# Performance work log

Hardware: AMD Instinct MI355X
Metric: run time of the kernel (lower is better)

## Reference

```python
import jax, jax.numpy as jnp
import numpy as np

N_NODES = 50000


def gcn_conv(x, edge_index, W, b, n_nodes):
    """GCNConv: out = D^-1/2 (A + I) D^-1/2 (x W) + b (symmetric norm, self-loops)."""
    src, dst = edge_index[0], edge_index[1]
    loop = jnp.arange(n_nodes, dtype=src.dtype)
    src = jnp.concatenate([src, loop])  # [E + N]
    dst = jnp.concatenate([dst, loop])
    deg = jax.ops.segment_sum(jnp.ones_like(dst, dtype=x.dtype), dst,
                              num_segments=n_nodes)
    dinv = jnp.where(deg > 0, jax.lax.rsqrt(deg), 0.0)
    norm = dinv[src] * dinv[dst]  # [E + N]
    h = x @ W  # [N, out_dim]
    msg = h[src] * norm[:, None]  # gather + scale, [E + N, out_dim]
    out = jax.ops.segment_sum(msg, dst, num_segments=n_nodes)  # scatter-add
    return out + b


def batch_norm(x, gamma, beta, eps=1e-5):
    mean = jnp.mean(x, axis=0)
    var = jnp.var(x, axis=0)
    return (x - mean) * jax.lax.rsqrt(var + eps) * gamma + beta


def setup_inputs() -> dict:
    key = jax.random.key(0)
    ks = jax.random.split(key, 6)
    in_c, hid, lat = 64, 128, 64
    x = jax.random.normal(ks[0], (N_NODES, in_c), dtype=jnp.float32)
    edge_index = jax.random.randint(ks[1], (2, 1600000), 0, N_NODES, dtype=jnp.int64)
    W1 = jax.random.normal(ks[2], (in_c, hid), dtype=jnp.float32) * (1.0 / np.sqrt(in_c))
    b1 = jnp.zeros((hid,), dtype=jnp.float32)
    gamma = jnp.ones((hid,), dtype=jnp.float32)
    beta = jnp.zeros((hid,), dtype=jnp.float32)
    W2 = jax.random.normal(ks[3], (hid, lat), dtype=jnp.float32) * (1.0 / np.sqrt(hid))
    b2 = jnp.zeros((lat,), dtype=jnp.float32)
    return {"x": x, "edge_index": edge_index, "W1": W1, "b1": b1,
            "gamma": gamma, "beta": beta, "W2": W2, "b2": b2}


def reference(x, edge_index, W1, b1, gamma, beta, W2, b2):
    h = gcn_conv(x, edge_index, W1, b1, N_NODES)
    h = batch_norm(h, gamma, beta)
    h = jax.nn.relu(h)
    # dropout omitted (deterministic reference; identity in expectation-free eval)
    return gcn_conv(h, edge_index, W2, b2, N_NODES)
```

## Files before the change

### kernel.cpp

```cpp
#include <hip/hip_runtime.h>

#define N_NODES 50000
#define C1 64
#define C2 128
#define C3 64
#define NBUCK ((N_NODES + 63) / 64)
#define BCAP 8192
#define STILE 4096

__device__ __forceinline__ float bf2f(unsigned short u) {
    union { unsigned int i; float f; } v; v.i = ((unsigned int)u) << 16; return v.f;
}
__device__ __forceinline__ unsigned short f2bf(float f) {
    union { float f; unsigned int i; } v; v.f = f;
    return (unsigned short)((v.i + 0x7FFFu + ((v.i >> 16) & 1u)) >> 16);
}

__global__ void k_zero_cast(const float* __restrict__ x, unsigned short* __restrict__ xh,
                            int* __restrict__ bcount, float* __restrict__ stats) {
    int i = blockIdx.x * blockDim.x + threadIdx.x;
    if (i < NBUCK) bcount[i] = 0;
    if (i < 512) stats[i] = 0.0f;
    if (i < N_NODES * C1 / 4) {
        float4 v = ((const float4*)x)[i];
        ushort4 o;
        o.x = f2bf(v.x); o.y = f2bf(v.y); o.z = f2bf(v.z); o.w = f2bf(v.w);
        ((ushort4*)xh)[i] = o;
    }
}

__global__ __launch_bounds__(256) void k_hist(const int* __restrict__ dst, int E,
                                              int* __restrict__ bcount) {
    __shared__ int lh[NBUCK];
    int tid = threadIdx.x;
    for (int i = tid; i < NBUCK; i += 256) lh[i] = 0;
    __syncthreads();
    int stride = gridDim.x * blockDim.x;
    for (int e = blockIdx.x * blockDim.x + tid; e < E; e += stride)
        atomicAdd(&lh[dst[e] >> 6], 1);
    __syncthreads();
    for (int i = tid; i < NBUCK; i += 256)
        if (lh[i]) atomicAdd(&bcount[i], lh[i]);
}

__global__ __launch_bounds__(1024) void k_scanb(const int* __restrict__ bcount,
                                                int* __restrict__ bstart,
                                                int* __restrict__ bcursor) {
    __shared__ int sums[1024];
    int t = threadIdx.x;
    int v = (t < NBUCK) ? bcount[t] : 0;
    sums[t] = v;
    __syncthreads();
    for (int off = 1; off < 1024; off <<= 1) {
        int u = (t >= off) ? sums[t - off] : 0;
        __syncthreads();
        sums[t] += u;
        __syncthreads();
    }
    if (t < NBUCK) {
        int ex = sums[t] - v;
        bstart[t] = ex;
        bcursor[t * 16] = ex;
    }
}

__global__ __launch_bounds__(256) void k_scatterc(const int* __restrict__ src,
                                                  const int* __restrict__ dst, int E,
                                                  int* __restrict__ bcursor,
                                                  int* __restrict__ pairs) {
    __shared__ int lh[NBUCK];
    __shared__ int gbase[NBUCK];
    int tid = threadIdx.x;
    int base = blockIdx.x * STILE;
    for (int i = tid; i < NBUCK; i += 256) lh[i] = 0;
    __syncthreads();
    int sv[16], dv[16], rk[16];
#pragma unroll
    for (int k = 0; k < 16; ++k) {
        int e = base + k * 256 + tid;
        sv[k] = -1;
        if (e < E) {
            sv[k] = src[e];
            dv[k] = dst[e];
            rk[k] = atomicAdd(&lh[dv[k] >> 6], 1);
        }
    }
    __syncthreads();
    for (int i = tid; i < NBUCK; i += 256) {
        int c = lh[i];
        gbase[i] = c ? atomicAdd(&bcursor[i * 16], c) : 0;
    }
    __syncthreads();
#pragma unroll
    for (int k = 0; k < 16; ++k) {
        if (sv[k] >= 0) {
            int b = dv[k] >> 6;
            pairs[gbase[b] + rk[k]] = (sv[k] << 6) | (dv[k] & 63);
        }
    }
}

__global__ __launch_bounds__(256) void k_refine(const int* __restrict__ bstart,
                                                const int* __restrict__ bcount,
                                                int* __restrict__ rowstart,
                                                float* __restrict__ dinv,
                                                int* __restrict__ pairs) {
    __shared__ int stage[BCAP];
    __shared__ int lcnt[64];
    __shared__ int lcur[64];
    int b = blockIdx.x;
    int tid = threadIdx.x;
    int e0 = bstart[b], n = bcount[b];
    if (tid < 64) lcnt[tid] = 0;
    __syncthreads();
    for (int j = tid; j < n; j += 256) {
        int pk = pairs[e0 + j];
        stage[j] = pk;
        atomicAdd(&lcnt[pk & 63], 1);
    }
    __syncthreads();
    if (tid < 64) {
        int dg = lcnt[tid];
        int pfx = dg;
#pragma unroll
        for (int off = 1; off < 64; off <<= 1) {
            int v = __shfl_up(pfx, off);
            if (tid >= off) pfx += v;
        }
        int st = e0 + (pfx - dg);
        int nd = b * 64 + tid;
        rowstart[nd] = st;
        dinv[nd] = rsqrtf(1.0f + (float)dg);
        lcur[tid] = st;
    }
    __syncthreads();
    for (int j = tid; j < n; j += 256) {
        int pk = stage[j];
        int pos = atomicAdd(&lcur[pk & 63], 1);
        pairs[pos] = pk >> 6;
    }
}

__global__ __launch_bounds__(256) void k_pullx(const int* __restrict__ rowstart,
                                               const int* __restrict__ csr,
                                               const float* __restrict__ x,
                                               const unsigned short* __restrict__ xh,
                                               const float* __restrict__ dinv,
                                               float* __restrict__ aggx) {
    int node = blockIdx.x * 4 + (threadIdx.x >> 6);
    if (node >= N_NODES) return;
    int lane = threadIdx.x & 63;
    int start = rowstart[node], end = rowstart[node + 1];
    float dd = dinv[node];
    float acc = x[node * C1 + lane] * dd * dd;
    for (int j0 = start; j0 < end; j0 += 64) {
        int n = end - j0; if (n > 64) n = 64;
        int idx = 0;
        if (lane < n) idx = csr[j0 + lane];
        float ds = dinv[idx];
        int k = 0;
        for (; k + 3 < n; k += 4) {
            int s0 = __shfl(idx, k),     s1 = __shfl(idx, k + 1);
            int s2 = __shfl(idx, k + 2), s3 = __shfl(idx, k + 3);
            float w0 = __shfl(ds, k) * dd,     w1 = __shfl(ds, k + 1) * dd;
            float w2 = __shfl(ds, k + 2) * dd, w3 = __shfl(ds, k + 3) * dd;
            float v0 = bf2f(xh[s0 * C1 + lane]), v1 = bf2f(xh[s1 * C1 + lane]);
            float v2 = bf2f(xh[s2 * C1 + lane]), v3 = bf2f(xh[s3 * C1 + lane]);
            acc = fmaf(v0, w0, acc); acc = fmaf(v1, w1, acc);
            acc = fmaf(v2, w2, acc); acc = fmaf(v3, w3, acc);
        }
        for (; k < n; ++k) {
            int s = __shfl(idx, k);
            float w = __shfl(ds, k) * dd;
            acc = fmaf(bf2f(xh[s * C1 + lane]), w, acc);
        }
    }
    aggx[node * C1 + lane] = acc;
}

__global__ __launch_bounds__(256) void k_gemm1b(const float* __restrict__ aggx,
                                                const float* __restrict__ W1,
                                                const float* __restrict__ b1,
                                                float* __restrict__ agg1) {
    __shared__ float Ws[C1 * C2];
    __shared__ float Xs[32 * C1];
    int tid = threadIdx.x;
    int r0 = blockIdx.x * 32;
    for (int i = tid; i < C1 * C2; i += 256) Ws[i] = W1[i];
    for (int i = tid; i < 32 * C1; i += 256) {
        int row = r0 + (i >> 6);
        Xs[i] = (row < N_NODES) ? aggx[row * C1 + (i & 63)] : 0.0f;
    }
    __syncthreads();
    int c = tid & 127;
    int rg = tid >> 7;
    float bv = b1[c];
    float acc[16];
#pragma unroll
    for (int r = 0; r < 16; ++r) acc[r] = 0.0f;
    for (int k = 0; k < C1; ++k) {
        float w = Ws[k * C2 + c];
#pragma unroll
        for (int r = 0; r < 16; ++r)
            acc[r] = fmaf(Xs[(rg * 16 + r) * C1 + k], w, acc[r]);
    }
#pragma unroll
    for (int r = 0; r < 16; ++r) {
        int row = r0 + rg * 16 + r;
        if (row < N_NODES) agg1[row * C2 + c] = acc[r] + bv;
    }
}

__global__ __launch_bounds__(256) void k_stats(const float* __restrict__ agg1,
                                               float* __restrict__ stats) {
    __shared__ float ls[256], lq[256];
    int tid = threadIdx.x;
    int c = tid & 127, half = tid >> 7;
    float s = 0.0f, q = 0.0f;
    for (int row = blockIdx.x * 2 + half; row < N_NODES; row += gridDim.x * 2) {
        float v = agg1[row * C2 + c];
        s += v; q += v * v;
    }
    ls[tid] = s; lq[tid] = q;
    __syncthreads();
    if (tid < 128) {
        s = ls[tid] + ls[tid + 128];
        q = lq[tid] + lq[tid + 128];
        unsafeAtomicAdd(&stats[c], s);
        unsafeAtomicAdd(&stats[128 + c], q);
    }
}

__global__ void k_bnparam(const float* __restrict__ gamma, const float* __restrict__ beta,
                          float* __restrict__ stats) {
    int c = threadIdx.x;
    if (c < 128) {
        const float invN = 1.0f / (float)N_NODES;
        float mean = stats[c] * invN;
        float var = stats[128 + c] * invN - mean * mean;
        float sc = gamma[c] * rsqrtf(var + 1e-5f);
        stats[256 + c] = sc;
        stats[384 + c] = beta[c] - mean * sc;
    }
}

__global__ __launch_bounds__(256) void k_gemm2(const float* __restrict__ agg1,
                                               const float* __restrict__ W2,
                                               const float* __restrict__ stats,
                                               unsigned short* __restrict__ h2h) {
    __shared__ float Ws[C2 * C3];
    __shared__ float As[32 * C2];
    int tid = threadIdx.x;
    int r0 = blockIdx.x * 32;
    for (int i = tid; i < C2 * C3; i += 256) Ws[i] = W2[i];
    for (int i = tid; i < 32 * C2; i += 256) {
        int row = r0 + (i >> 7);
        int cc = i & 127;
        float v = 0.0f;
        if (row < N_NODES)
            v = fmaxf(fmaf(agg1[row * C2 + cc], stats[256 + cc], stats[384 + cc]), 0.0f);
        As[i] = v;
    }
    __syncthreads();
    int c = tid & 63;
    int rg = tid >> 6;
    float acc[8];
#pragma unroll
    for (int r = 0; r < 8; ++r) acc[r] = 0.0f;
    for (int k = 0; k < C2; ++k) {
        float w = Ws[k * C3 + c];
#pragma unroll
        for (int r = 0; r < 8; ++r)
            acc[r] = fmaf(As[(rg * 8 + r) * C2 + k], w, acc[r]);
    }
#pragma unroll
    for (int r = 0; r < 8; ++r) {
        int row = r0 + rg * 8 + r;
        if (row < N_NODES) h2h[row * C3 + c] = f2bf(acc[r]);
    }
}

__global__ __launch_bounds__(256) void k_pull2(const int* __restrict__ rowstart,
                                               const int* __restrict__ csr,
                                               const unsigned short* __restrict__ h2h,
                                               const float* __restrict__ dinv,
                                               const float* __restrict__ b2,
                                               float* __restrict__ out) {
    int node = blockIdx.x * 4 + (threadIdx.x >> 6);
    if (node >= N_NODES) return;
    int lane = threadIdx.x & 63;
    int start = rowstart[node], end = rowstart[node + 1];
    float dd = dinv[node];
    float acc = fmaf(bf2f(h2h[node * C3 + lane]), dd * dd, b2[lane]);
    for (int j0 = start; j0 < end; j0 += 64) {
        int n = end - j0; if (n > 64) n = 64;
        int idx = 0;
        if (lane < n) idx = csr[j0 + lane];
        float ds = dinv[idx];
        int k = 0;
        for (; k + 3 < n; k += 4) {
            int s0 = __shfl(idx, k),     s1 = __shfl(idx, k + 1);
            int s2 = __shfl(idx, k + 2), s3 = __shfl(idx, k + 3);
            float w0 = __shfl(ds, k) * dd,     w1 = __shfl(ds, k + 1) * dd;
            float w2 = __shfl(ds, k + 2) * dd, w3 = __shfl(ds, k + 3) * dd;
            float v0 = bf2f(h2h[s0 * C3 + lane]), v1 = bf2f(h2h[s1 * C3 + lane]);
            float v2 = bf2f(h2h[s2 * C3 + lane]), v3 = bf2f(h2h[s3 * C3 + lane]);
            acc = fmaf(v0, w0, acc); acc = fmaf(v1, w1, acc);
            acc = fmaf(v2, w2, acc); acc = fmaf(v3, w3, acc);
        }
        for (; k < n; ++k) {
            int s = __shfl(idx, k);
            float w = __shfl(ds, k) * dd;
            acc = fmaf(bf2f(h2h[s * C3 + lane]), w, acc);
        }
    }
    out[node * C3 + lane] = acc;
}

extern "C" void kernel_launch(void* const* d_in, const int* in_sizes, int n_in,
                              void* d_out, int out_size, void* d_ws, size_t ws_size,
                              hipStream_t stream) {
    const float* x     = (const float*)d_in[0];
    const int*   ei    = (const int*)d_in[1];
    const float* W1    = (const float*)d_in[2];
    const float* b1    = (const float*)d_in[3];
    const float* gamma = (const float*)d_in[4];
    const float* beta  = (const float*)d_in[5];
    const float* W2    = (const float*)d_in[6];
    const float* b2    = (const float*)d_in[7];
    float* out = (float*)d_out;

    int E = in_sizes[1] / 2;
    const int* src = ei;
    const int* dst = ei + E;

    char* ws = (char*)d_ws;
    float*          dinv     = (float*)ws;
    float*          stats    = (float*)(ws + 200704);
    int*            bcount   = (int*)(ws + 202752);
    int*            bstart   = (int*)(ws + 206848);
    int*            bcursor  = (int*)(ws + 210944);
    int*            rowstart = (int*)(ws + 261120);
    int*            pairs    = (int*)(ws + 461824);
    unsigned short* xh       = (unsigned short*)(ws + 6861824);
    float*          aggx     = (float*)(ws + 13261824);
    float*          agg1     = (float*)(ws + 26061824);
    unsigned short* h2h      = (unsigned short*)(ws + 51661824);

    const int nblk_cast  = (N_NODES * C1 / 4 + 255) / 256;
    const int nblk_rows  = (N_NODES + 31) / 32;
    const int nblk_scat  = (E + STILE - 1) / STILE;
    const int nblk_pull  = (N_NODES + 3) / 4;

    k_zero_cast<<<nblk_cast, 256, 0, stream>>>(x, xh, bcount, stats);
    k_hist<<<256, 256, 0, stream>>>(dst, E, bcount);
    k_scanb<<<1, 1024, 0, stream>>>(bcount, bstart, bcursor);
    k_scatterc<<<nblk_scat, 256, 0, stream>>>(src, dst, E, bcursor, pairs);
    k_refine<<<NBUCK, 256, 0, stream>>>(bstart, bcount, rowstart, dinv, pairs);

    k_pullx<<<nblk_pull, 256, 0, stream>>>(rowstart, pairs, x, xh, dinv, aggx);
    k_gemm1b<<<nblk_rows, 256, 0, stream>>>(aggx, W1, b1, agg1);

    k_stats<<<256, 256, 0, stream>>>(agg1, stats);
    k_bnparam<<<1, 128, 0, stream>>>(gamma, beta, stats);

    k_gemm2<<<nblk_rows, 256, 0, stream>>>(agg1, W2, stats, h2h);
    k_pull2<<<nblk_pull, 256, 0, stream>>>(rowstart, pairs, h2h, dinv, b2, out);
}
```

Before: 319.9 us.

## Pack bf16 source degree weight with node index into CSR entries

Adds a pass that packs each CSR entry's source index (low 16 bits) with the bf16 of that source's dinv (high 16 bits), and rewrites both aggregation kernels to read these packed words directly. The old per-chunk lane load, dinv gather and shuffle broadcast are replaced by uniform scalar loads with four independent accumulators. This removes the dependent dinv gather and the shuffles from the hot loops, at the cost of an extra edge-length kernel and buffer. It also reduces edge weight precision to bf16. Source indices must fit in 16 bits, but N_NODES is 50000, so they do.

```diff
diff --git a/kernel.cpp b/kernel.cpp
--- a/kernel.cpp
+++ b/kernel.cpp
@@ -14,6 +14,9 @@
 __device__ __forceinline__ unsigned short f2bf(float f) {
     union { float f; unsigned int i; } v; v.f = f;
     return (unsigned short)((v.i + 0x7FFFu + ((v.i >> 16) & 1u)) >> 16);
+}
+__device__ __forceinline__ float hi2f(unsigned int p) {
+    union { unsigned int i; float f; } v; v.i = p & 0xFFFF0000u; return v.f;
 }
 
 __global__ void k_zero_cast(const float* __restrict__ x, unsigned short* __restrict__ xh,
@@ -141,8 +144,17 @@
     }
 }
 
+__global__ void k_pack(const int* __restrict__ csr, const float* __restrict__ dinv,
+                       unsigned int* __restrict__ wsrc, int E) {
+    int j = blockIdx.x * blockDim.x + threadIdx.x;
+    if (j < E) {
+        int s = csr[j];
+        wsrc[j] = ((unsigned int)f2bf(dinv[s]) << 16) | (unsigned int)s;
+    }
+}
+
 __global__ __launch_bounds__(256) void k_pullx(const int* __restrict__ rowstart,
-                                               const int* __restrict__ csr,
+                                               const unsigned int* __restrict__ wsrc,
                                                const float* __restrict__ x,
                                                const unsigned short* __restrict__ xh,
                                                const float* __restrict__ dinv,
@@ -152,30 +164,24 @@
     int lane = threadIdx.x & 63;
     int start = rowstart[node], end = rowstart[node + 1];
     float dd = dinv[node];
-    float acc = x[node * C1 + lane] * dd * dd;
-    for (int j0 = start; j0 < end; j0 += 64) {
-        int n = end - j0; if (n > 64) n = 64;
-        int idx = 0;
-        if (lane < n) idx = csr[j0 + lane];
-        float ds = dinv[idx];
-        int k = 0;
-        for (; k + 3 < n; k += 4) {
-            int s0 = __shfl(idx, k),     s1 = __shfl(idx, k + 1);
-            int s2 = __shfl(idx, k + 2), s3 = __shfl(idx, k + 3);
-            float w0 = __shfl(ds, k) * dd,     w1 = __shfl(ds, k + 1) * dd;
-            float w2 = __shfl(ds, k + 2) * dd, w3 = __shfl(ds, k + 3) * dd;
-            float v0 = bf2f(xh[s0 * C1 + lane]), v1 = bf2f(xh[s1 * C1 + lane]);
-            float v2 = bf2f(xh[s2 * C1 + lane]), v3 = bf2f(xh[s3 * C1 + lane]);
-            acc = fmaf(v0, w0, acc); acc = fmaf(v1, w1, acc);
-            acc = fmaf(v2, w2, acc); acc = fmaf(v3, w3, acc);
-        }
-        for (; k < n; ++k) {
-            int s = __shfl(idx, k);
-            float w = __shfl(ds, k) * dd;
-            acc = fmaf(bf2f(xh[s * C1 + lane]), w, acc);
-        }
-    }
-    aggx[node * C1 + lane] = acc;
+    float a0 = 0.0f, a1 = 0.0f, a2 = 0.0f, a3 = 0.0f;
+    int j = start;
+    for (; j + 3 < end; j += 4) {
+        unsigned int p0 = wsrc[j],     p1 = wsrc[j + 1];
+        unsigned int p2 = wsrc[j + 2], p3 = wsrc[j + 3];
+        float v0 = bf2f(xh[(p0 & 0xFFFFu) * C1 + lane]);
+        float v1 = bf2f(xh[(p1 & 0xFFFFu) * C1 + lane]);
+        float v2 = bf2f(xh[(p2 & 0xFFFFu) * C1 + lane]);
+        float v3 = bf2f(xh[(p3 & 0xFFFFu) * C1 + lane]);
+        a0 = fmaf(v0, hi2f(p0), a0); a1 = fmaf(v1, hi2f(p1), a1);
+        a2 = fmaf(v2, hi2f(p2), a2); a3 = fmaf(v3, hi2f(p3), a3);
+    }
+    for (; j < end; ++j) {
+        unsigned int p = wsrc[j];
+        a0 = fmaf(bf2f(xh[(p & 0xFFFFu) * C1 + lane]), hi2f(p), a0);
+    }
+    float eacc = (a0 + a1) + (a2 + a3);
+    aggx[node * C1 + lane] = fmaf(x[node * C1 + lane], dd * dd, dd * eacc);
 }
 
 __global__ __launch_bounds__(256) void k_gemm1b(const float* __restrict__ aggx,
@@ -281,7 +287,7 @@
 }
 
 __global__ __launch_bounds__(256) void k_pull2(const int* __restrict__ rowstart,
-                                               const int* __restrict__ csr,
+                                               const unsigned int* __restrict__ wsrc,
                                                const unsigned short* __restrict__ h2h,
                                                const float* __restrict__ dinv,
                                                const float* __restrict__ b2,
@@ -291,30 +297,25 @@
     int lane = threadIdx.x & 63;
     int start = rowstart[node], end = rowstart[node + 1];
     float dd = dinv[node];
-    float acc = fmaf(bf2f(h2h[node * C3 + lane]), dd * dd, b2[lane]);
-    for (int j0 = start; j0 < end; j0 += 64) {
-        int n = end - j0; if (n > 64) n = 64;
-        int idx = 0;
-        if (lane < n) idx = csr[j0 + lane];
-        float ds = dinv[idx];
-        int k = 0;
-        for (; k + 3 < n; k += 4) {
-            int s0 = __shfl(idx, k),     s1 = __shfl(idx, k + 1);
-            int s2 = __shfl(idx, k + 2), s3 = __shfl(idx, k + 3);
-            float w0 = __shfl(ds, k) * dd,     w1 = __shfl(ds, k + 1) * dd;
-            float w2 = __shfl(ds, k + 2) * dd, w3 = __shfl(ds, k + 3) * dd;
-            float v0 = bf2f(h2h[s0 * C3 + lane]), v1 = bf2f(h2h[s1 * C3 + lane]);
-            float v2 = bf2f(h2h[s2 * C3 + lane]), v3 = bf2f(h2h[s3 * C3 + lane]);
-            acc = fmaf(v0, w0, acc); acc = fmaf(v1, w1, acc);
-            acc = fmaf(v2, w2, acc); acc = fmaf(v3, w3, acc);
-        }
-        for (; k < n; ++k) {
-            int s = __shfl(idx, k);
-            float w = __shfl(ds, k) * dd;
-            acc = fmaf(bf2f(h2h[s * C3 + lane]), w, acc);
-        }
-    }
-    out[node * C3 + lane] = acc;
+    float a0 = 0.0f, a1 = 0.0f, a2 = 0.0f, a3 = 0.0f;
+    int j = start;
+    for (; j + 3 < end; j += 4) {
+        unsigned int p0 = wsrc[j],     p1 = wsrc[j + 1];
+        unsigned int p2 = wsrc[j + 2], p3 = wsrc[j + 3];
+        float v0 = bf2f(h2h[(p0 & 0xFFFFu) * C3 + lane]);
+        float v1 = bf2f(h2h[(p1 & 0xFFFFu) * C3 + lane]);
+        float v2 = bf2f(h2h[(p2 & 0xFFFFu) * C3 + lane]);
+        float v3 = bf2f(h2h[(p3 & 0xFFFFu) * C3 + lane]);
+        a0 = fmaf(v0, hi2f(p0), a0); a1 = fmaf(v1, hi2f(p1), a1);
+        a2 = fmaf(v2, hi2f(p2), a2); a3 = fmaf(v3, hi2f(p3), a3);
+    }
+    for (; j < end; ++j) {
+        unsigned int p = wsrc[j];
+        a0 = fmaf(bf2f(h2h[(p & 0xFFFFu) * C3 + lane]), hi2f(p), a0);
+    }
+    float eacc = (a0 + a1) + (a2 + a3);
+    float self = bf2f(h2h[node * C3 + lane]);
+    out[node * C3 + lane] = b2[lane] + fmaf(self, dd * dd, dd * eacc);
 }
 
 extern "C" void kernel_launch(void* const* d_in, const int* in_sizes, int n_in,
@@ -342,14 +343,16 @@
     int*            bcursor  = (int*)(ws + 210944);
     int*            rowstart = (int*)(ws + 261120);
     int*            pairs    = (int*)(ws + 461824);
-    unsigned short* xh       = (unsigned short*)(ws + 6861824);
-    float*          aggx     = (float*)(ws + 13261824);
-    float*          agg1     = (float*)(ws + 26061824);
-    unsigned short* h2h      = (unsigned short*)(ws + 51661824);
+    unsigned int*   wsrc     = (unsigned int*)(ws + 6861824);
+    unsigned short* xh       = (unsigned short*)(ws + 13261824);
+    float*          aggx     = (float*)(ws + 19661824);
+    float*          agg1     = (float*)(ws + 32461824);
+    unsigned short* h2h      = (unsigned short*)(ws + 58061824);
 
     const int nblk_cast  = (N_NODES * C1 / 4 + 255) / 256;
     const int nblk_rows  = (N_NODES + 31) / 32;
     const int nblk_scat  = (E + STILE - 1) / STILE;
+    const int nblk_edge  = (E + 255) / 256;
     const int nblk_pull  = (N_NODES + 3) / 4;
 
     k_zero_cast<<<nblk_cast, 256, 0, stream>>>(x, xh, bcount, stats);
@@ -357,13 +360,14 @@
     k_scanb<<<1, 1024, 0, stream>>>(bcount, bstart, bcursor);
     k_scatterc<<<nblk_scat, 256, 0, stream>>>(src, dst, E, bcursor, pairs);
     k_refine<<<NBUCK, 256, 0, stream>>>(bstart, bcount, rowstart, dinv, pairs);
-
-    k_pullx<<<nblk_pull, 256, 0, stream>>>(rowstart, pairs, x, xh, dinv, aggx);
+    k_pack<<<nblk_edge, 256, 0, stream>>>(pairs, dinv, wsrc, E);
+
+    k_pullx<<<nblk_pull, 256, 0, stream>>>(rowstart, wsrc, x, xh, dinv, aggx);
     k_gemm1b<<<nblk_rows, 256, 0, stream>>>(aggx, W1, b1, agg1);
 
     k_stats<<<256, 256, 0, stream>>>(agg1, stats);
     k_bnparam<<<1, 128, 0, stream>>>(gamma, beta, stats);
 
     k_gemm2<<<nblk_rows, 256, 0, stream>>>(agg1, W2, stats, h2h);
-    k_pull2<<<nblk_pull, 256, 0, stream>>>(rowstart, pairs, h2h, dinv, b2, out);
-}
+    k_pull2<<<nblk_pull, 256, 0, stream>>>(rowstart, wsrc, h2h, dinv, b2, out);
+}
```

After: 349.3 us. 9.2% more time.
